# Kernel optimization log

Hardware: AMD Instinct MI355X
Metric: run time of the kernel (lower is better)

## Reference

```python
import jax, jax.numpy as jnp
import numpy as np

B, S, D, FD = 2, 2048, 1024, 4096
EPS_LN = 1e-5


def _l2norm(x):
    n = jnp.linalg.norm(x, axis=-1, keepdims=True)
    return x / jnp.maximum(n, 1e-12)


def _layernorm(x, w, b):
    m = x.mean(-1, keepdims=True)
    v = ((x - m) ** 2).mean(-1, keepdims=True)
    return (x - m) / jnp.sqrt(v + EPS_LN) * w + b


def _spl(x, mu_w, mu_b, gate, proto):
    # cosine-similarity gated linear (SparseProtoLinear)
    scores = _l2norm(x) @ _l2norm(proto).T          # [..., out]
    rw = jax.nn.relu(scores - gate)
    comp = x @ mu_w.T + mu_b
    return comp * rw


def _rotate_half(x):
    h = x.shape[-1] // 2
    return jnp.concatenate([-x[..., h:], x[..., :h]], axis=-1)


def _forward(x, cos, sin,
             ln1_w, ln1_b, ln2_w, ln2_b,
             qkv_mu, qkv_proto, qkv_bias, qkv_gate,
             o_mu, o_proto, o_bias, o_gate,
             f1_mu, f1_proto, f1_bias, f1_gate,
             f2_mu, f2_proto, f2_bias, f2_gate,
             pt_qkv, pt_o, pt_f1, pt_f2,
             pln_qkv_w, pln_qkv_b, pln_o_w, pln_o_b,
             pln_f1_w, pln_f1_b, pln_f2_w, pln_f2_b,
             prev_qkv, prev_o, prev_f1, prev_f2):
    # effective protos: proto_weight + LN(Linear(prev_proto))
    eff_qkv = qkv_proto + _layernorm(prev_qkv @ pt_qkv.T, pln_qkv_w, pln_qkv_b)
    eff_o   = o_proto   + _layernorm(prev_o   @ pt_o.T,   pln_o_w,   pln_o_b)
    eff_f1  = f1_proto  + _layernorm(prev_f1  @ pt_f1.T,  pln_f1_w,  pln_f1_b)
    eff_f2  = f2_proto  + _layernorm(prev_f2  @ pt_f2.T,  pln_f2_w,  pln_f2_b)

    # attention
    attn_in = _layernorm(x, ln1_w, ln1_b)
    m_qkv = _spl(attn_in, qkv_mu, qkv_bias, qkv_gate, eff_qkv)   # [B,S,3D]
    q, k, v = jnp.split(m_qkv, 3, axis=-1)
    c = cos[None]; s = sin[None]
    q = q * c + _rotate_half(q) * s
    k = k * c + _rotate_half(k) * s
    scale = 1.0 / jnp.sqrt(jnp.asarray(D, x.dtype))
    scores = jnp.einsum('bqd,bkd->bqk', q, k) * scale            # [B,S,S]
    causal = jnp.tril(jnp.ones((S, S), dtype=bool))
    scores = jnp.where(causal[None], scores, jnp.finfo(x.dtype).min)
    attn = jax.nn.softmax(scores, axis=-1)
    attn_out = jnp.einsum('bqk,bkd->bqd', attn, v)
    m_o = _spl(attn_out, o_mu, o_bias, o_gate, eff_o)
    x1 = x + m_o

    # ffn (DynamicInfiniteExpert)
    ffn_in = _layernorm(x1, ln2_w, ln2_b)
    m1 = _spl(ffn_in, f1_mu, f1_bias, f1_gate, eff_f1)           # [B,S,FD]
    h = jax.nn.relu(m1)
    m2 = _spl(h, f2_mu, f2_bias, f2_gate, eff_f2)                # [B,S,D]
    return x1 + m2


def setup_inputs() -> dict:
    key = jax.random.key(0)
    ks = iter(jax.random.split(key, 64))

    def nrm(shape, scale=1.0):
        return jax.random.normal(next(ks), shape, dtype=jnp.float32) * scale

    # RoPE tables
    pos = np.arange(S, dtype=np.float32)
    inv_freq = 1.0 / (10000.0 ** (np.arange(0, D, 2, dtype=np.float32) / D))
    freqs = np.outer(pos, inv_freq)
    emb = np.concatenate([freqs, freqs], axis=-1)
    cos = jnp.asarray(np.cos(emb)); sin = jnp.asarray(np.sin(emb))

    sD = 1.0 / np.sqrt(D); sF = 1.0 / np.sqrt(FD)
    inp = {
        'x': nrm((B, S, D)), 'cos': cos, 'sin': sin,
        'ln1_w': jnp.ones((D,)), 'ln1_b': jnp.zeros((D,)),
        'ln2_w': jnp.ones((D,)), 'ln2_b': jnp.zeros((D,)),
        'qkv_mu': nrm((3 * D, D), sD), 'qkv_proto': nrm((3 * D, D), sD),
        'qkv_bias': jnp.zeros((3 * D,)), 'qkv_gate': jnp.zeros((3 * D,)),
        'o_mu': nrm((D, D), sD), 'o_proto': nrm((D, D), sD),
        'o_bias': jnp.zeros((D,)), 'o_gate': jnp.zeros((D,)),
        'f1_mu': nrm((FD, D), sD), 'f1_proto': nrm((FD, D), sD),
        'f1_bias': jnp.zeros((FD,)), 'f1_gate': jnp.zeros((FD,)),
        'f2_mu': nrm((D, FD), sF), 'f2_proto': nrm((D, FD), sF),
        'f2_bias': jnp.zeros((D,)), 'f2_gate': jnp.zeros((D,)),
        'pt_qkv': nrm((D, D), sD), 'pt_o': nrm((D, D), sD),
        'pt_f1': nrm((D, D), sD), 'pt_f2': nrm((FD, FD), sF),
        'pln_qkv_w': jnp.ones((D,)), 'pln_qkv_b': jnp.zeros((D,)),
        'pln_o_w': jnp.ones((D,)), 'pln_o_b': jnp.zeros((D,)),
        'pln_f1_w': jnp.ones((D,)), 'pln_f1_b': jnp.zeros((D,)),
        'pln_f2_w': jnp.ones((FD,)), 'pln_f2_b': jnp.zeros((FD,)),
        'prev_qkv': nrm((3 * D, D), sD), 'prev_o': nrm((D, D), sD),
        'prev_f1': nrm((FD, D), sD), 'prev_f2': nrm((D, FD), sF),
    }
    return inp


def reference(x, cos, sin,
              ln1_w, ln1_b, ln2_w, ln2_b,
              qkv_mu, qkv_proto, qkv_bias, qkv_gate,
              o_mu, o_proto, o_bias, o_gate,
              f1_mu, f1_proto, f1_bias, f1_gate,
              f2_mu, f2_proto, f2_bias, f2_gate,
              pt_qkv, pt_o, pt_f1, pt_f2,
              pln_qkv_w, pln_qkv_b, pln_o_w, pln_o_b,
              pln_f1_w, pln_f1_b, pln_f2_w, pln_f2_b,
              prev_qkv, prev_o, prev_f1, prev_f2):
    return _forward(x, cos, sin, ln1_w, ln1_b, ln2_w, ln2_b,
                    qkv_mu, qkv_proto, qkv_bias, qkv_gate,
                    o_mu, o_proto, o_bias, o_gate,
                    f1_mu, f1_proto, f1_bias, f1_gate,
                    f2_mu, f2_proto, f2_bias, f2_gate,
                    pt_qkv, pt_o, pt_f1, pt_f2,
                    pln_qkv_w, pln_qkv_b, pln_o_w, pln_o_b,
                    pln_f1_w, pln_f1_b, pln_f2_w, pln_f2_b,
                    prev_qkv, prev_o, prev_f1, prev_f2)
```

## Files before the change

### kernel.cpp

```cpp
#include <hip/hip_runtime.h>
#include <cstdint>

typedef unsigned short u16;
typedef __attribute__((ext_vector_type(8))) short sh8;
typedef __attribute__((ext_vector_type(4))) float f32x4;

struct __align__(8) us4 { u16 x, y, z, w; };

__device__ __forceinline__ u16 f2bf(float f) {
  unsigned u = __float_as_uint(f);
  u += 0x7FFFu + ((u >> 16) & 1u);
  return (u16)(u >> 16);
}
__device__ __forceinline__ float bf2f(u16 h) {
  return __uint_as_float((unsigned)h << 16);
}

__device__ __forceinline__ float blk_sum(float v, float* red) {
#pragma unroll
  for (int o = 32; o; o >>= 1) v += __shfl_xor(v, o);
  __syncthreads();
  if ((threadIdx.x & 63) == 0) red[threadIdx.x >> 6] = v;
  __syncthreads();
  return red[0] + red[1] + red[2] + red[3];
}
__device__ __forceinline__ float blk_max(float v, float* red) {
#pragma unroll
  for (int o = 32; o; o >>= 1) v = fmaxf(v, __shfl_xor(v, o));
  __syncthreads();
  if ((threadIdx.x & 63) == 0) red[threadIdx.x >> 6] = v;
  __syncthreads();
  return fmaxf(fmaxf(red[0], red[1]), fmaxf(red[2], red[3]));
}

__global__ void cvt_bf16(const float* __restrict__ S, u16* __restrict__ D, long n4) {
  long i = (long)blockIdx.x * blockDim.x + threadIdx.x;
  if (i >= n4) return;
  float4 v = ((const float4*)S)[i];
  us4 o; o.x = f2bf(v.x); o.y = f2bf(v.y); o.z = f2bf(v.z); o.w = f2bf(v.w);
  ((us4*)D)[i] = o;
}

__global__ void fillv(float* __restrict__ o, long n, float v) {
  long i = (long)blockIdx.x * blockDim.x + threadIdx.x;
  if (i < n) o[i] = v;
}

template <typename CT>
__global__ __launch_bounds__(256, 2) void gemm_bt(
    const u16* __restrict__ A, const u16* __restrict__ B, CT* __restrict__ C,
    int M, int N, int K, int lda, int ldb,
    int mode, long zsA, long zsB, long zsC) {
  int bm, bn;
  int z = blockIdx.z;
  if (mode == 3) {
    int t = blockIdx.x;
    int m = (int)floorf((sqrtf(8.f * t + 1.f) - 1.f) * 0.5f);
    while ((m + 1) * (m + 2) / 2 <= t) ++m;
    while (m * (m + 1) / 2 > t) --m;
    bm = m; bn = t - m * (m + 1) / 2;
  } else {
    bm = blockIdx.x; bn = blockIdx.y;
  }
  int k0s = 0, k0e = K;
  if (mode == 1) {
    int kc = K / gridDim.z;
    k0s = z * kc; k0e = k0s + kc;
    C += (size_t)z * M * (size_t)N;
  } else if (mode >= 2) {
    A += (size_t)z * zsA; B += (size_t)z * zsB; C += (size_t)z * zsC;
  }

  __shared__ __align__(16) u16 As[128 * 32];
  __shared__ __align__(16) u16 Bs[128 * 32];
  int tid = threadIdx.x, wid = tid >> 6, lane = tid & 63;
  int wr = (wid >> 1) << 6, wc = (wid & 1) << 6;
  int lr = lane & 15, lk = (lane >> 4) << 3;

  f32x4 acc[4][4];
  const f32x4 zf = {0.f, 0.f, 0.f, 0.f};
#pragma unroll
  for (int i = 0; i < 4; ++i)
#pragma unroll
    for (int j = 0; j < 4; ++j) acc[i][j] = zf;

  int r0 = tid >> 2, c0 = (tid & 3) << 3;
  const size_t baseA = (size_t)bm * 128, baseB = (size_t)bn * 128;
  const u16* Ab = A + baseA * lda;
  const u16* Bp = B + baseB * ldb;

  for (int k0 = k0s; k0 < k0e; k0 += 32) {
    __builtin_amdgcn_global_load_lds(
        (const __attribute__((address_space(1))) void*)(Ab + (size_t)r0 * lda + k0 + c0),
        (__attribute__((address_space(3))) void*)(As + (wid << 9)), 16, 0, 0);
    __builtin_amdgcn_global_load_lds(
        (const __attribute__((address_space(1))) void*)(Ab + (size_t)(64 + r0) * lda + k0 + c0),
        (__attribute__((address_space(3))) void*)(As + 2048 + (wid << 9)), 16, 0, 0);
    __builtin_amdgcn_global_load_lds(
        (const __attribute__((address_space(1))) void*)(Bp + (size_t)r0 * ldb + k0 + c0),
        (__attribute__((address_space(3))) void*)(Bs + (wid << 9)), 16, 0, 0);
    __builtin_amdgcn_global_load_lds(
        (const __attribute__((address_space(1))) void*)(Bp + (size_t)(64 + r0) * ldb + k0 + c0),
        (__attribute__((address_space(3))) void*)(Bs + 2048 + (wid << 9)), 16, 0, 0);
    __syncthreads();
    sh8 af[4], bfr[4];
#pragma unroll
    for (int f = 0; f < 4; ++f) {
      af[f]  = *(const sh8*)(As + (wr + f * 16 + lr) * 32 + lk);
      bfr[f] = *(const sh8*)(Bs + (wc + f * 16 + lr) * 32 + lk);
    }
#pragma unroll
    for (int i = 0; i < 4; ++i)
#pragma unroll
      for (int j = 0; j < 4; ++j)
        acc[i][j] = __builtin_amdgcn_mfma_f32_16x16x32_bf16(af[i], bfr[j], acc[i][j], 0, 0, 0);
    __syncthreads();
  }

  int cr = (lane >> 4) << 2, cc = lane & 15;
#pragma unroll
  for (int i = 0; i < 4; ++i)
#pragma unroll
    for (int j = 0; j < 4; ++j) {
      size_t cb = (baseA + wr + i * 16 + cr) * (size_t)N + (baseB + wc + j * 16 + cc);
#pragma unroll
      for (int r = 0; r < 4; ++r) {
        float v = acc[i][j][r];
        if constexpr (sizeof(CT) == 2) C[cb + (size_t)r * N] = (CT)f2bf(v);
        else                           C[cb + (size_t)r * N] = v;
      }
    }
}

__global__ void ln_rows(const float* __restrict__ X, const float* __restrict__ w,
                        const float* __restrict__ b, u16* __restrict__ Y,
                        float* __restrict__ norms, int C) {
  __shared__ float red[4];
  int row = blockIdx.x;
  const float* x = X + (size_t)row * C;
  int nv = C >> 2;
  float s = 0.f, ss = 0.f;
  for (int i = threadIdx.x; i < nv; i += 256) {
    float4 v = ((const float4*)x)[i];
    s += v.x + v.y + v.z + v.w;
    ss += v.x * v.x + v.y * v.y + v.z * v.z + v.w * v.w;
  }
  s = blk_sum(s, red);
  ss = blk_sum(ss, red);
  float mean = s / C;
  float inv = rsqrtf(fmaxf(ss / C - mean * mean, 0.f) + 1e-5f);
  float nrm = 0.f;
  for (int i = threadIdx.x; i < nv; i += 256) {
    float4 v = ((const float4*)x)[i];
    float4 wv = ((const float4*)w)[i];
    float4 bv = ((const float4*)b)[i];
    float y0 = (v.x - mean) * inv * wv.x + bv.x;
    float y1 = (v.y - mean) * inv * wv.y + bv.y;
    float y2 = (v.z - mean) * inv * wv.z + bv.z;
    float y3 = (v.w - mean) * inv * wv.w + bv.w;
    nrm += y0 * y0 + y1 * y1 + y2 * y2 + y3 * y3;
    us4 o; o.x = f2bf(y0); o.y = f2bf(y1); o.z = f2bf(y2); o.w = f2bf(y3);
    ((us4*)(Y + (size_t)row * C))[i] = o;
  }
  nrm = blk_sum(nrm, red);
  if (threadIdx.x == 0) norms[row] = fmaxf(sqrtf(nrm), 1e-12f);
}

__global__ void ln_add_norm(const float* __restrict__ T0, const float* __restrict__ T1,
                            const float* __restrict__ P,
                            const float* __restrict__ w, const float* __restrict__ b,
                            u16* __restrict__ E, float* __restrict__ norms, int C) {
  __shared__ float red[4];
  int row = blockIdx.x;
  const float* t0 = T0 + (size_t)row * C;
  const float* t1 = T1 ? T1 + (size_t)row * C : nullptr;
  const float* p = P + (size_t)row * C;
  int nv = C >> 2;
  float s = 0.f, ss = 0.f;
  for (int i = threadIdx.x; i < nv; i += 256) {
    float4 v = ((const float4*)t0)[i];
    if (t1) {
      float4 v1 = ((const float4*)t1)[i];
      v.x += v1.x; v.y += v1.y; v.z += v1.z; v.w += v1.w;
    }
    s += v.x + v.y + v.z + v.w;
    ss += v.x * v.x + v.y * v.y + v.z * v.z + v.w * v.w;
  }
  s = blk_sum(s, red);
  ss = blk_sum(ss, red);
  float mean = s / C;
  float inv = rsqrtf(fmaxf(ss / C - mean * mean, 0.f) + 1e-5f);
  float nrm = 0.f;
  for (int i = threadIdx.x; i < nv; i += 256) {
    float4 v = ((const float4*)t0)[i];
    if (t1) {
      float4 v1 = ((const float4*)t1)[i];
      v.x += v1.x; v.y += v1.y; v.z += v1.z; v.w += v1.w;
    }
    float4 pv = ((const float4*)p)[i];
    float4 wv = ((const float4*)w)[i];
    float4 bv = ((const float4*)b)[i];
    float y0 = pv.x + (v.x - mean) * inv * wv.x + bv.x;
    float y1 = pv.y + (v.y - mean) * inv * wv.y + bv.y;
    float y2 = pv.z + (v.z - mean) * inv * wv.z + bv.z;
    float y3 = pv.w + (v.w - mean) * inv * wv.w + bv.w;
    nrm += y0 * y0 + y1 * y1 + y2 * y2 + y3 * y3;
    us4 o; o.x = f2bf(y0); o.y = f2bf(y1); o.z = f2bf(y2); o.w = f2bf(y3);
    ((us4*)(E + (size_t)row * C))[i] = o;
  }
  nrm = blk_sum(nrm, red);
  if (threadIdx.x == 0) norms[row] = fmaxf(sqrtf(nrm), 1e-12f);
}

__global__ void rownorm_bf(const u16* __restrict__ X, float* __restrict__ norms, int C) {
  __shared__ float red[4];
  int row = blockIdx.x;
  const us4* x = (const us4*)(X + (size_t)row * C);
  int nv = C >> 2;
  float nrm = 0.f;
  for (int i = threadIdx.x; i < nv; i += 256) {
    us4 v = x[i];
    float a = bf2f(v.x), b = bf2f(v.y), c = bf2f(v.z), d = bf2f(v.w);
    nrm += a * a + b * b + c * c + d * d;
  }
  nrm = blk_sum(nrm, red);
  if (threadIdx.x == 0) norms[row] = fmaxf(sqrtf(nrm), 1e-12f);
}

template <typename OT>
__global__ void spl_epi_b(const u16* __restrict__ G, const float* __restrict__ bias,
                          const float* __restrict__ gate, const float* __restrict__ rn,
                          const float* __restrict__ cn, const float* __restrict__ resid,
                          OT* __restrict__ out, int C, int relu_out) {
  int r = blockIdx.x;
  int c = (blockIdx.y << 10) + (threadIdx.x << 2);
  const u16* gr = G + (size_t)r * (2 * C);
  us4 cv = *(const us4*)(gr + c);
  us4 dv = *(const us4*)(gr + C + c);
  float4 bv = *(const float4*)(bias + c);
  float4 gv = *(const float4*)(gate + c);
  float4 nv = *(const float4*)(cn + c);
  float rr = rn[r];
  float cf[4] = {bf2f(cv.x), bf2f(cv.y), bf2f(cv.z), bf2f(cv.w)};
  float df[4] = {bf2f(dv.x), bf2f(dv.y), bf2f(dv.z), bf2f(dv.w)};
  float bb[4] = {bv.x, bv.y, bv.z, bv.w};
  float gg[4] = {gv.x, gv.y, gv.z, gv.w};
  float nn[4] = {nv.x, nv.y, nv.z, nv.w};
  float o[4];
#pragma unroll
  for (int j = 0; j < 4; ++j) {
    float sc = df[j] / (rr * nn[j]);
    float v = (cf[j] + bb[j]) * fmaxf(sc - gg[j], 0.f);
    if (relu_out) v = fmaxf(v, 0.f);
    o[j] = v;
  }
  if (resid) {
    float4 rv = *(const float4*)(resid + (size_t)r * C + c);
    o[0] += rv.x; o[1] += rv.y; o[2] += rv.z; o[3] += rv.w;
  }
  if constexpr (sizeof(OT) == 2) {
    us4 ov; ov.x = f2bf(o[0]); ov.y = f2bf(o[1]); ov.z = f2bf(o[2]); ov.w = f2bf(o[3]);
    *(us4*)((u16*)out + (size_t)r * C + c) = ov;
  } else {
    float4 ov = {o[0], o[1], o[2], o[3]};
    *(float4*)((float*)out + (size_t)r * C + c) = ov;
  }
}

__global__ void spl_epi_p(const float* __restrict__ G0, const float* __restrict__ G1,
                          const float* __restrict__ bias, const float* __restrict__ gate,
                          const float* __restrict__ rn, const float* __restrict__ cn,
                          const float* __restrict__ resid, float* __restrict__ out,
                          int C) {
  int r = blockIdx.x;
  int c = (blockIdx.y << 10) + (threadIdx.x << 2);
  size_t rowb = (size_t)r * (2 * C);
  float4 c0 = *(const float4*)(G0 + rowb + c);
  float4 c1 = *(const float4*)(G1 + rowb + c);
  float4 d0 = *(const float4*)(G0 + rowb + C + c);
  float4 d1 = *(const float4*)(G1 + rowb + C + c);
  float4 bv = *(const float4*)(bias + c);
  float4 gv = *(const float4*)(gate + c);
  float4 nv = *(const float4*)(cn + c);
  float4 rv = *(const float4*)(resid + (size_t)r * C + c);
  float rr = rn[r];
  float cf[4] = {c0.x + c1.x, c0.y + c1.y, c0.z + c1.z, c0.w + c1.w};
  float df[4] = {d0.x + d1.x, d0.y + d1.y, d0.z + d1.z, d0.w + d1.w};
  float bb[4] = {bv.x, bv.y, bv.z, bv.w};
  float gg[4] = {gv.x, gv.y, gv.z, gv.w};
  float nn[4] = {nv.x, nv.y, nv.z, nv.w};
  float re[4] = {rv.x, rv.y, rv.z, rv.w};
  float4 ov;
  float* op = (float*)&ov;
#pragma unroll
  for (int j = 0; j < 4; ++j) {
    float sc = df[j] / (rr * nn[j]);
    op[j] = (cf[j] + bb[j]) * fmaxf(sc - gg[j], 0.f) + re[j];
  }
  *(float4*)(out + (size_t)r * C + c) = ov;
}

__global__ void rope_ip(u16* __restrict__ MQ, const float* __restrict__ CT_,
                        const float* __restrict__ ST_) {
  long t = (long)blockIdx.x * blockDim.x + threadIdx.x;
  int i = (int)(t & 511);
  long row = t >> 9;
  int s = (int)(row & 2047);
  u16* base = MQ + row * 3072;
  float c0 = CT_[(size_t)s * 1024 + i], c1 = CT_[(size_t)s * 1024 + 512 + i];
  float s0 = ST_[(size_t)s * 1024 + i], s1 = ST_[(size_t)s * 1024 + 512 + i];
  float q0 = bf2f(base[i]), q1 = bf2f(base[512 + i]);
  base[i]        = f2bf(q0 * c0 - q1 * s0);
  base[512 + i]  = f2bf(q1 * c1 + q0 * s1);
  float k0 = bf2f(base[1024 + i]), k1 = bf2f(base[1536 + i]);
  base[1024 + i] = f2bf(k0 * c0 - k1 * s0);
  base[1536 + i] = f2bf(k1 * c1 + k0 * s1);
}

__global__ void vtrans(const u16* __restrict__ MQ, u16* __restrict__ VT) {
  __shared__ u16 tile[32][33];
  int b = blockIdx.z;
  int s0 = blockIdx.x << 5, d0 = blockIdx.y << 5;
  int tx = threadIdx.x, ty = threadIdx.y;
  for (int r = ty; r < 32; r += 8)
    tile[r][tx] = MQ[((size_t)(b * 2048 + s0 + r)) * 3072 + 2048 + d0 + tx];
  __syncthreads();
  for (int r = ty; r < 32; r += 8)
    VT[(size_t)b * 1024 * 2048 + (size_t)(d0 + r) * 2048 + s0 + tx] = tile[tx][r];
}

__global__ void softmax_causal(const float* __restrict__ S, u16* __restrict__ P) {
  __shared__ float red[4];
  int b = blockIdx.x >> 11;
  int q = blockIdx.x & 2047;
  const float* row = S + ((size_t)b << 22) + (size_t)q * 2048;
  u16* prow = P + ((size_t)b << 22) + (size_t)q * 2048;
  int nv = q + 1;
  int base = threadIdx.x * 8;
  float xv[8];
  float4 a = *(const float4*)(row + base);
  float4 bq = *(const float4*)(row + base + 4);
  xv[0] = a.x; xv[1] = a.y; xv[2] = a.z; xv[3] = a.w;
  xv[4] = bq.x; xv[5] = bq.y; xv[6] = bq.z; xv[7] = bq.w;
  float m = -3.4e38f;
#pragma unroll
  for (int j = 0; j < 8; ++j) {
    xv[j] *= 0.03125f;
    if (base + j < nv) m = fmaxf(m, xv[j]);
  }
  m = blk_max(m, red);
  float e[8];
  float ssum = 0.f;
#pragma unroll
  for (int j = 0; j < 8; ++j) {
    e[j] = (base + j < nv) ? __expf(xv[j] - m) : 0.f;
    ssum += e[j];
  }
  ssum = blk_sum(ssum, red);
  float invs = 1.f / ssum;
  us4 o;
  o.x = f2bf(e[0] * invs); o.y = f2bf(e[1] * invs);
  o.z = f2bf(e[2] * invs); o.w = f2bf(e[3] * invs);
  ((us4*)prow)[threadIdx.x * 2] = o;
  o.x = f2bf(e[4] * invs); o.y = f2bf(e[5] * invs);
  o.z = f2bf(e[6] * invs); o.w = f2bf(e[7] * invs);
  ((us4*)prow)[threadIdx.x * 2 + 1] = o;
}

extern "C" void kernel_launch(void* const* d_in, const int* in_sizes, int n_in,
                              void* d_out, int out_size, void* d_ws, size_t ws_size,
                              hipStream_t stream) {
  (void)in_sizes;
  const float* x         = (const float*)d_in[0];
  const float* cosT      = (const float*)d_in[1];
  const float* sinT      = (const float*)d_in[2];
  const float* ln1_w     = (const float*)d_in[3];
  const float* ln1_b     = (const float*)d_in[4];
  const float* ln2_w     = (const float*)d_in[5];
  const float* ln2_b     = (const float*)d_in[6];
  const float* qkv_mu    = (const float*)d_in[7];
  const float* qkv_proto = (const float*)d_in[8];
  const float* qkv_bias  = (const float*)d_in[9];
  const float* qkv_gate  = (const float*)d_in[10];
  const float* o_mu      = (const float*)d_in[11];
  const float* o_proto   = (const float*)d_in[12];
  const float* o_bias    = (const float*)d_in[13];
  const float* o_gate    = (const float*)d_in[14];
  const float* f1_mu     = (const float*)d_in[15];
  const float* f1_proto  = (const float*)d_in[16];
  const float* f1_bias   = (const float*)d_in[17];
  const float* f1_gate   = (const float*)d_in[18];
  const float* f2_mu     = (const float*)d_in[19];
  const float* f2_proto  = (const float*)d_in[20];
  const float* f2_bias   = (const float*)d_in[21];
  const float* f2_gate   = (const float*)d_in[22];
  const float* pt_qkv    = (const float*)d_in[23];
  const float* pt_o      = (const float*)d_in[24];
  const float* pt_f1     = (const float*)d_in[25];
  const float* pt_f2     = (const float*)d_in[26];
  const float* pln_qkv_w = (const float*)d_in[27];
  const float* pln_qkv_b = (const float*)d_in[28];
  const float* pln_o_w   = (const float*)d_in[29];
  const float* pln_o_b   = (const float*)d_in[30];
  const float* pln_f1_w  = (const float*)d_in[31];
  const float* pln_f1_b  = (const float*)d_in[32];
  const float* pln_f2_w  = (const float*)d_in[33];
  const float* pln_f2_b  = (const float*)d_in[34];
  const float* prev_qkv  = (const float*)d_in[35];
  const float* prev_o    = (const float*)d_in[36];
  const float* prev_f1   = (const float*)d_in[37];
  const float* prev_f2   = (const float*)d_in[38];

  const long D = 1024, TD = 3072, FD = 4096, R = 4096;

  char* W = (char*)d_ws;
  size_t off = 0;
  auto alloc = [&](size_t bytes) {
    void* p = W + off;
    off = (off + bytes + 255) & ~(size_t)255;
    return p;
  };
  char* GOUT = (char*)alloc(67108864);
  u16*  RC   = (u16*)alloc(33554432);
  u16*  wq   = (u16*)alloc(2 * TD * D * 2);
  u16*  wo   = (u16*)alloc(2 * D * D * 2);
  u16*  wf1  = (u16*)alloc(2 * FD * D * 2);
  u16*  wf2  = (u16*)alloc(2 * D * FD * 2);
  float* X1  = (float*)alloc(R * D * 4);
  float* SC  = (float*)alloc(R * D * 4);
  u16*  P1   = (u16*)alloc(R * D * 2);
  u16*  VT   = (u16*)alloc(2 * D * 2048 * 2);
  u16*  AOB  = (u16*)alloc(R * D * 2);
  float* pnq     = (float*)alloc(TD * 4);
  float* pno     = (float*)alloc(D * 4);
  float* pnf1    = (float*)alloc(FD * 4);
  float* pnf2    = (float*)alloc(D * 4);
  float* rn_ain  = (float*)alloc(R * 4);
  float* rn_aout = (float*)alloc(R * 4);
  float* rn_ffn  = (float*)alloc(R * 4);
  float* rn_h    = (float*)alloc(R * 4);
  size_t need = off;

  if (n_in < 39 || need > ws_size) {
    long n = out_size;
    fillv<<<dim3((unsigned)((n + 255) / 256)), 256, 0, stream>>>((float*)d_out, n, 12345.0f);
    return;
  }

  u16* SA = (u16*)GOUT;
  u16* SB = (u16*)(GOUT + 33554432);
  float* SCORES = (float*)GOUT;
  u16* PB = (u16*)(GOUT + 33554432);

  auto cvt = [&](const float* s, u16* d, long n) {
    long n4 = n >> 2;
    cvt_bf16<<<dim3((unsigned)((n4 + 255) / 256)), 256, 0, stream>>>(s, d, n4);
  };

  struct Proto { const float* prev; const float* pt; const float* proto;
                 const float* w; const float* b; u16* wbuf; float* pn;
                 int M; int N; int K; };
  Proto protos[4] = {
    {prev_qkv, pt_qkv, qkv_proto, pln_qkv_w, pln_qkv_b, wq,  pnq,  3072, 1024, 1024},
    {prev_o,   pt_o,   o_proto,   pln_o_w,   pln_o_b,   wo,  pno,  1024, 1024, 1024},
    {prev_f1,  pt_f1,  f1_proto,  pln_f1_w,  pln_f1_b,  wf1, pnf1, 4096, 1024, 1024},
    {prev_f2,  pt_f2,  f2_proto,  pln_f2_w,  pln_f2_b,  wf2, pnf2, 1024, 4096, 4096},
  };
  for (int p = 0; p < 4; ++p) {
    Proto& pr = protos[p];
    u16* eff = pr.wbuf + (size_t)pr.M * pr.N;
    cvt(pr.prev, SA, (long)pr.M * pr.K);
    cvt(pr.pt,   SB, (long)pr.N * pr.K);
    if (pr.K == 4096) {
      float* T0 = (float*)RC;
      float* T1 = T0 + (size_t)pr.M * pr.N;
      gemm_bt<float><<<dim3(pr.M / 128, pr.N / 128, 2), 256, 0, stream>>>(
          SA, SB, T0, pr.M, pr.N, pr.K, pr.K, pr.K, 1, 0, 0, 0);
      ln_add_norm<<<pr.M, 256, 0, stream>>>(T0, T1, pr.proto, pr.w, pr.b, eff, pr.pn, pr.N);
    } else {
      gemm_bt<float><<<dim3(pr.M / 128, pr.N / 128, 1), 256, 0, stream>>>(
          SA, SB, SC, pr.M, pr.N, pr.K, pr.K, pr.K, 0, 0, 0, 0);
      ln_add_norm<<<pr.M, 256, 0, stream>>>(SC, nullptr, pr.proto, pr.w, pr.b, eff, pr.pn, pr.N);
    }
  }
  cvt(qkv_mu, wq, TD * D);
  cvt(o_mu,   wo, D * D);
  cvt(f1_mu,  wf1, FD * D);
  cvt(f2_mu,  wf2, D * FD);

  ln_rows<<<4096, 256, 0, stream>>>(x, ln1_w, ln1_b, P1, rn_ain, 1024);
  gemm_bt<u16><<<dim3(32, 48, 1), 256, 0, stream>>>(
      P1, wq, (u16*)GOUT, 4096, 6144, 1024, 1024, 1024, 0, 0, 0, 0);
  spl_epi_b<u16><<<dim3(4096, 3), 256, 0, stream>>>(
      (u16*)GOUT, qkv_bias, qkv_gate, rn_ain, pnq, nullptr, RC, 3072, 0);

  rope_ip<<<dim3((unsigned)((R * 512) / 256)), 256, 0, stream>>>(RC, cosT, sinT);
  vtrans<<<dim3(64, 32, 2), dim3(32, 8), 0, stream>>>(RC, VT);
  gemm_bt<float><<<dim3(136, 1, 2), 256, 0, stream>>>(
      RC, RC + 1024, SCORES, 2048, 2048, 1024, 3072, 3072,
      3, 2048L * 3072, 2048L * 3072, 1L << 22);
  softmax_causal<<<4096, 256, 0, stream>>>(SCORES, PB);
  gemm_bt<u16><<<dim3(16, 8, 2), 256, 0, stream>>>(
      PB, VT, AOB, 2048, 1024, 2048, 2048, 2048,
      2, 1L << 22, 1024L * 2048, 2048L * 1024);
  rownorm_bf<<<4096, 256, 0, stream>>>(AOB, rn_aout, 1024);

  gemm_bt<u16><<<dim3(32, 16, 1), 256, 0, stream>>>(
      AOB, wo, (u16*)GOUT, 4096, 2048, 1024, 1024, 1024, 0, 0, 0, 0);
  spl_epi_b<float><<<dim3(4096, 1), 256, 0, stream>>>(
      (u16*)GOUT, o_bias, o_gate, rn_aout, pno, x, X1, 1024, 0);

  ln_rows<<<4096, 256, 0, stream>>>(X1, ln2_w, ln2_b, P1, rn_ffn, 1024);
  gemm_bt<u16><<<dim3(32, 64, 1), 256, 0, stream>>>(
      P1, wf1, (u16*)GOUT, 4096, 8192, 1024, 1024, 1024, 0, 0, 0, 0);
  spl_epi_b<u16><<<dim3(4096, 4), 256, 0, stream>>>(
      (u16*)GOUT, f1_bias, f1_gate, rn_ffn, pnf1, nullptr, RC, 4096, 1);
  rownorm_bf<<<4096, 256, 0, stream>>>(RC, rn_h, 4096);
  gemm_bt<float><<<dim3(32, 16, 2), 256, 0, stream>>>(
      RC, wf2, (float*)GOUT, 4096, 2048, 4096, 4096, 4096, 1, 0, 0, 0);
  spl_epi_p<<<dim3(4096, 1), 256, 0, stream>>>(
      (float*)GOUT, (float*)GOUT + 4096L * 2048, f2_bias, f2_gate, rn_h, pnf2,
      X1, (float*)d_out, 1024);
}
```

Measured before the change: 663.1 us.

## Fuse SPL epilogues with RoPE/LN/rownorm, batch proto GEMMs, skip causal zero blocks

Several changes land together. The QKV epilogue now applies RoPE directly, the O epilogue is fused with the residual add and LN2, and the F1 epilogue computes the row norm. The three K=1024 proto GEMMs are batched into one ragged launch (mode 5), and their intermediate outputs, plus the split-K partials, are stored in bf16 rather than fp32. Causal PV skips the zero K tiles (mode 4), and softmax stops reading and writing masked regions. Together these cut launches and memory traffic, at the cost of some precision from bf16 partial sums.

```diff
diff --git a/kernel.cpp b/kernel.cpp
--- a/kernel.cpp
+++ b/kernel.cpp
@@ -67,8 +67,15 @@
     int kc = K / gridDim.z;
     k0s = z * kc; k0e = k0s + kc;
     C += (size_t)z * M * (size_t)N;
-  } else if (mode >= 2) {
+  } else if (mode == 2 || mode == 3) {
     A += (size_t)z * zsA; B += (size_t)z * zsB; C += (size_t)z * zsC;
+  } else if (mode == 4) {
+    A += (size_t)z * zsA; B += (size_t)z * zsB; C += (size_t)z * zsC;
+    k0e = (bm + 1) * 128;
+  } else if (mode == 5) {
+    int Mz = (int)((zsB >> (z * 16)) & 0xFFFF);
+    if (bm * 128 >= Mz) return;
+    A += (size_t)z * zsA; B += (size_t)z * 1048576; C += (size_t)z * zsC;
   }
 
   __shared__ __align__(16) u16 As[128 * 32];
@@ -166,25 +173,26 @@
   if (threadIdx.x == 0) norms[row] = fmaxf(sqrtf(nrm), 1e-12f);
 }
 
-__global__ void ln_add_norm(const float* __restrict__ T0, const float* __restrict__ T1,
+__global__ void ln_add_norm(const u16* __restrict__ T0, const u16* __restrict__ T1,
                             const float* __restrict__ P,
                             const float* __restrict__ w, const float* __restrict__ b,
                             u16* __restrict__ E, float* __restrict__ norms, int C) {
   __shared__ float red[4];
   int row = blockIdx.x;
-  const float* t0 = T0 + (size_t)row * C;
-  const float* t1 = T1 ? T1 + (size_t)row * C : nullptr;
+  const us4* t0 = (const us4*)(T0 + (size_t)row * C);
+  const us4* t1 = T1 ? (const us4*)(T1 + (size_t)row * C) : nullptr;
   const float* p = P + (size_t)row * C;
   int nv = C >> 2;
   float s = 0.f, ss = 0.f;
   for (int i = threadIdx.x; i < nv; i += 256) {
-    float4 v = ((const float4*)t0)[i];
+    us4 v = t0[i];
+    float f0 = bf2f(v.x), f1 = bf2f(v.y), f2 = bf2f(v.z), f3 = bf2f(v.w);
     if (t1) {
-      float4 v1 = ((const float4*)t1)[i];
-      v.x += v1.x; v.y += v1.y; v.z += v1.z; v.w += v1.w;
+      us4 v1 = t1[i];
+      f0 += bf2f(v1.x); f1 += bf2f(v1.y); f2 += bf2f(v1.z); f3 += bf2f(v1.w);
     }
-    s += v.x + v.y + v.z + v.w;
-    ss += v.x * v.x + v.y * v.y + v.z * v.z + v.w * v.w;
+    s += f0 + f1 + f2 + f3;
+    ss += f0 * f0 + f1 * f1 + f2 * f2 + f3 * f3;
   }
   s = blk_sum(s, red);
   ss = blk_sum(ss, red);
@@ -192,18 +200,19 @@
   float inv = rsqrtf(fmaxf(ss / C - mean * mean, 0.f) + 1e-5f);
   float nrm = 0.f;
   for (int i = threadIdx.x; i < nv; i += 256) {
-    float4 v = ((const float4*)t0)[i];
+    us4 v = t0[i];
+    float f0 = bf2f(v.x), f1 = bf2f(v.y), f2 = bf2f(v.z), f3 = bf2f(v.w);
     if (t1) {
-      float4 v1 = ((const float4*)t1)[i];
-      v.x += v1.x; v.y += v1.y; v.z += v1.z; v.w += v1.w;
+      us4 v1 = t1[i];
+      f0 += bf2f(v1.x); f1 += bf2f(v1.y); f2 += bf2f(v1.z); f3 += bf2f(v1.w);
     }
     float4 pv = ((const float4*)p)[i];
     float4 wv = ((const float4*)w)[i];
     float4 bv = ((const float4*)b)[i];
-    float y0 = pv.x + (v.x - mean) * inv * wv.x + bv.x;
-    float y1 = pv.y + (v.y - mean) * inv * wv.y + bv.y;
-    float y2 = pv.z + (v.z - mean) * inv * wv.z + bv.z;
-    float y3 = pv.w + (v.w - mean) * inv * wv.w + bv.w;
+    float y0 = pv.x + (f0 - mean) * inv * wv.x + bv.x;
+    float y1 = pv.y + (f1 - mean) * inv * wv.y + bv.y;
+    float y2 = pv.z + (f2 - mean) * inv * wv.z + bv.z;
+    float y3 = pv.w + (f3 - mean) * inv * wv.w + bv.w;
     nrm += y0 * y0 + y1 * y1 + y2 * y2 + y3 * y3;
     us4 o; o.x = f2bf(y0); o.y = f2bf(y1); o.z = f2bf(y2); o.w = f2bf(y3);
     ((us4*)(E + (size_t)row * C))[i] = o;
@@ -227,65 +236,154 @@
   if (threadIdx.x == 0) norms[row] = fmaxf(sqrtf(nrm), 1e-12f);
 }
 
-template <typename OT>
-__global__ void spl_epi_b(const u16* __restrict__ G, const float* __restrict__ bias,
-                          const float* __restrict__ gate, const float* __restrict__ rn,
-                          const float* __restrict__ cn, const float* __restrict__ resid,
-                          OT* __restrict__ out, int C, int relu_out) {
-  int r = blockIdx.x;
-  int c = (blockIdx.y << 10) + (threadIdx.x << 2);
-  const u16* gr = G + (size_t)r * (2 * C);
+__device__ __forceinline__ void epi4(const u16* gr, int C, int c, float rr,
+                                     const float* bias, const float* gate,
+                                     const float* cn, float* o) {
   us4 cv = *(const us4*)(gr + c);
   us4 dv = *(const us4*)(gr + C + c);
   float4 bv = *(const float4*)(bias + c);
   float4 gv = *(const float4*)(gate + c);
   float4 nv = *(const float4*)(cn + c);
-  float rr = rn[r];
   float cf[4] = {bf2f(cv.x), bf2f(cv.y), bf2f(cv.z), bf2f(cv.w)};
   float df[4] = {bf2f(dv.x), bf2f(dv.y), bf2f(dv.z), bf2f(dv.w)};
   float bb[4] = {bv.x, bv.y, bv.z, bv.w};
   float gg[4] = {gv.x, gv.y, gv.z, gv.w};
   float nn[4] = {nv.x, nv.y, nv.z, nv.w};
-  float o[4];
 #pragma unroll
   for (int j = 0; j < 4; ++j) {
     float sc = df[j] / (rr * nn[j]);
-    float v = (cf[j] + bb[j]) * fmaxf(sc - gg[j], 0.f);
-    if (relu_out) v = fmaxf(v, 0.f);
-    o[j] = v;
-  }
-  if (resid) {
-    float4 rv = *(const float4*)(resid + (size_t)r * C + c);
-    o[0] += rv.x; o[1] += rv.y; o[2] += rv.z; o[3] += rv.w;
-  }
-  if constexpr (sizeof(OT) == 2) {
+    o[j] = (cf[j] + bb[j]) * fmaxf(sc - gg[j], 0.f);
+  }
+}
+
+__global__ void spl_rope_row(const u16* __restrict__ G, const float* __restrict__ bias,
+                             const float* __restrict__ gate, const float* __restrict__ rn,
+                             const float* __restrict__ cn, const float* __restrict__ CT_,
+                             const float* __restrict__ ST_, u16* __restrict__ MQ) {
+  int r = blockIdx.x;
+  int s = r & 2047;
+  const u16* gr = G + (size_t)r * 6144;
+  u16* outr = MQ + (size_t)r * 3072;
+  float rr = rn[r];
+  int t = threadIdx.x;
+
+  int qk = (t >> 7);
+  int c = qk * 1024 + ((t & 127) << 2);
+  int d = c - qk * 1024;
+  float a0[4], a1[4];
+  epi4(gr, 3072, c, rr, bias, gate, cn, a0);
+  epi4(gr, 3072, c + 512, rr, bias, gate, cn, a1);
+  const float* ct = CT_ + (size_t)s * 1024;
+  const float* st = ST_ + (size_t)s * 1024;
+  float4 c0 = *(const float4*)(ct + d);
+  float4 s0 = *(const float4*)(st + d);
+  float4 c1 = *(const float4*)(ct + d + 512);
+  float4 s1 = *(const float4*)(st + d + 512);
+  float cc0[4] = {c0.x, c0.y, c0.z, c0.w}, ss0[4] = {s0.x, s0.y, s0.z, s0.w};
+  float cc1[4] = {c1.x, c1.y, c1.z, c1.w}, ss1[4] = {s1.x, s1.y, s1.z, s1.w};
+  us4 o0, o1;
+  o0.x = f2bf(a0[0] * cc0[0] - a1[0] * ss0[0]);
+  o0.y = f2bf(a0[1] * cc0[1] - a1[1] * ss0[1]);
+  o0.z = f2bf(a0[2] * cc0[2] - a1[2] * ss0[2]);
+  o0.w = f2bf(a0[3] * cc0[3] - a1[3] * ss0[3]);
+  o1.x = f2bf(a1[0] * cc1[0] + a0[0] * ss1[0]);
+  o1.y = f2bf(a1[1] * cc1[1] + a0[1] * ss1[1]);
+  o1.z = f2bf(a1[2] * cc1[2] + a0[2] * ss1[2]);
+  o1.w = f2bf(a1[3] * cc1[3] + a0[3] * ss1[3]);
+  *(us4*)(outr + c) = o0;
+  *(us4*)(outr + c + 512) = o1;
+
+  int cv_ = 2048 + (t << 2);
+  float vv[4];
+  epi4(gr, 3072, cv_, rr, bias, gate, cn, vv);
+  us4 ov; ov.x = f2bf(vv[0]); ov.y = f2bf(vv[1]); ov.z = f2bf(vv[2]); ov.w = f2bf(vv[3]);
+  *(us4*)(outr + cv_) = ov;
+}
+
+__global__ void spl_f1_row(const u16* __restrict__ G, const float* __restrict__ bias,
+                           const float* __restrict__ gate, const float* __restrict__ rn,
+                           const float* __restrict__ cn, u16* __restrict__ H,
+                           float* __restrict__ rn_h) {
+  __shared__ float red[4];
+  int r = blockIdx.x;
+  const u16* gr = G + (size_t)r * 8192;
+  u16* hr = H + (size_t)r * 4096;
+  float rr = rn[r];
+  float nrm = 0.f;
+  for (int c = threadIdx.x << 2; c < 4096; c += 1024) {
+    float o[4];
+    epi4(gr, 4096, c, rr, bias, gate, cn, o);
+#pragma unroll
+    for (int j = 0; j < 4; ++j) {
+      o[j] = fmaxf(o[j], 0.f);
+      nrm += o[j] * o[j];
+    }
     us4 ov; ov.x = f2bf(o[0]); ov.y = f2bf(o[1]); ov.z = f2bf(o[2]); ov.w = f2bf(o[3]);
-    *(us4*)((u16*)out + (size_t)r * C + c) = ov;
-  } else {
-    float4 ov = {o[0], o[1], o[2], o[3]};
-    *(float4*)((float*)out + (size_t)r * C + c) = ov;
-  }
-}
-
-__global__ void spl_epi_p(const float* __restrict__ G0, const float* __restrict__ G1,
+    *(us4*)(hr + c) = ov;
+  }
+  nrm = blk_sum(nrm, red);
+  if (threadIdx.x == 0) rn_h[r] = fmaxf(sqrtf(nrm), 1e-12f);
+}
+
+__global__ void spl_o_ln_row(const u16* __restrict__ G, const float* __restrict__ bias,
+                             const float* __restrict__ gate, const float* __restrict__ rn,
+                             const float* __restrict__ cn, const float* __restrict__ xres,
+                             const float* __restrict__ lw, const float* __restrict__ lb,
+                             float* __restrict__ X1, u16* __restrict__ Y,
+                             float* __restrict__ rn_ffn) {
+  __shared__ float red[4];
+  int r = blockIdx.x;
+  int c = threadIdx.x << 2;
+  const u16* gr = G + (size_t)r * 2048;
+  float o[4];
+  epi4(gr, 1024, c, rn[r], bias, gate, cn, o);
+  float4 rv = *(const float4*)(xres + (size_t)r * 1024 + c);
+  o[0] += rv.x; o[1] += rv.y; o[2] += rv.z; o[3] += rv.w;
+  float4 xo = {o[0], o[1], o[2], o[3]};
+  *(float4*)(X1 + (size_t)r * 1024 + c) = xo;
+  float s = o[0] + o[1] + o[2] + o[3];
+  float ss = o[0] * o[0] + o[1] * o[1] + o[2] * o[2] + o[3] * o[3];
+  s = blk_sum(s, red);
+  ss = blk_sum(ss, red);
+  float mean = s * (1.f / 1024.f);
+  float inv = rsqrtf(fmaxf(ss * (1.f / 1024.f) - mean * mean, 0.f) + 1e-5f);
+  float4 wv = *(const float4*)(lw + c);
+  float4 bv = *(const float4*)(lb + c);
+  float ww[4] = {wv.x, wv.y, wv.z, wv.w}, bb[4] = {bv.x, bv.y, bv.z, bv.w};
+  float nrm = 0.f;
+  us4 ov;
+  u16* op = (u16*)&ov;
+#pragma unroll
+  for (int j = 0; j < 4; ++j) {
+    float y = (o[j] - mean) * inv * ww[j] + bb[j];
+    nrm += y * y;
+    op[j] = f2bf(y);
+  }
+  *(us4*)(Y + (size_t)r * 1024 + c) = ov;
+  nrm = blk_sum(nrm, red);
+  if (threadIdx.x == 0) rn_ffn[r] = fmaxf(sqrtf(nrm), 1e-12f);
+}
+
+__global__ void spl_epi_p(const u16* __restrict__ G0, const u16* __restrict__ G1,
                           const float* __restrict__ bias, const float* __restrict__ gate,
                           const float* __restrict__ rn, const float* __restrict__ cn,
-                          const float* __restrict__ resid, float* __restrict__ out,
-                          int C) {
+                          const float* __restrict__ resid, float* __restrict__ out) {
   int r = blockIdx.x;
-  int c = (blockIdx.y << 10) + (threadIdx.x << 2);
-  size_t rowb = (size_t)r * (2 * C);
-  float4 c0 = *(const float4*)(G0 + rowb + c);
-  float4 c1 = *(const float4*)(G1 + rowb + c);
-  float4 d0 = *(const float4*)(G0 + rowb + C + c);
-  float4 d1 = *(const float4*)(G1 + rowb + C + c);
+  int c = threadIdx.x << 2;
+  size_t rowb = (size_t)r * 2048;
+  us4 c0 = *(const us4*)(G0 + rowb + c);
+  us4 c1 = *(const us4*)(G1 + rowb + c);
+  us4 d0 = *(const us4*)(G0 + rowb + 1024 + c);
+  us4 d1 = *(const us4*)(G1 + rowb + 1024 + c);
   float4 bv = *(const float4*)(bias + c);
   float4 gv = *(const float4*)(gate + c);
   float4 nv = *(const float4*)(cn + c);
-  float4 rv = *(const float4*)(resid + (size_t)r * C + c);
+  float4 rv = *(const float4*)(resid + (size_t)r * 1024 + c);
   float rr = rn[r];
-  float cf[4] = {c0.x + c1.x, c0.y + c1.y, c0.z + c1.z, c0.w + c1.w};
-  float df[4] = {d0.x + d1.x, d0.y + d1.y, d0.z + d1.z, d0.w + d1.w};
+  float cf[4] = {bf2f(c0.x) + bf2f(c1.x), bf2f(c0.y) + bf2f(c1.y),
+                 bf2f(c0.z) + bf2f(c1.z), bf2f(c0.w) + bf2f(c1.w)};
+  float df[4] = {bf2f(d0.x) + bf2f(d1.x), bf2f(d0.y) + bf2f(d1.y),
+                 bf2f(d0.z) + bf2f(d1.z), bf2f(d0.w) + bf2f(d1.w)};
   float bb[4] = {bv.x, bv.y, bv.z, bv.w};
   float gg[4] = {gv.x, gv.y, gv.z, gv.w};
   float nn[4] = {nv.x, nv.y, nv.z, nv.w};
@@ -297,24 +395,7 @@
     float sc = df[j] / (rr * nn[j]);
     op[j] = (cf[j] + bb[j]) * fmaxf(sc - gg[j], 0.f) + re[j];
   }
-  *(float4*)(out + (size_t)r * C + c) = ov;
-}
-
-__global__ void rope_ip(u16* __restrict__ MQ, const float* __restrict__ CT_,
-                        const float* __restrict__ ST_) {
-  long t = (long)blockIdx.x * blockDim.x + threadIdx.x;
-  int i = (int)(t & 511);
-  long row = t >> 9;
-  int s = (int)(row & 2047);
-  u16* base = MQ + row * 3072;
-  float c0 = CT_[(size_t)s * 1024 + i], c1 = CT_[(size_t)s * 1024 + 512 + i];
-  float s0 = ST_[(size_t)s * 1024 + i], s1 = ST_[(size_t)s * 1024 + 512 + i];
-  float q0 = bf2f(base[i]), q1 = bf2f(base[512 + i]);
-  base[i]        = f2bf(q0 * c0 - q1 * s0);
-  base[512 + i]  = f2bf(q1 * c1 + q0 * s1);
-  float k0 = bf2f(base[1024 + i]), k1 = bf2f(base[1536 + i]);
-  base[1024 + i] = f2bf(k0 * c0 - k1 * s0);
-  base[1536 + i] = f2bf(k1 * c1 + k0 * s1);
+  *(float4*)(out + (size_t)r * 1024 + c) = ov;
 }
 
 __global__ void vtrans(const u16* __restrict__ MQ, u16* __restrict__ VT) {
@@ -336,35 +417,41 @@
   const float* row = S + ((size_t)b << 22) + (size_t)q * 2048;
   u16* prow = P + ((size_t)b << 22) + (size_t)q * 2048;
   int nv = q + 1;
+  int wcap = ((q >> 7) + 1) << 7;
   int base = threadIdx.x * 8;
+  float e[8];
+  float m = -3.4e38f;
   float xv[8];
-  float4 a = *(const float4*)(row + base);
-  float4 bq = *(const float4*)(row + base + 4);
-  xv[0] = a.x; xv[1] = a.y; xv[2] = a.z; xv[3] = a.w;
-  xv[4] = bq.x; xv[5] = bq.y; xv[6] = bq.z; xv[7] = bq.w;
-  float m = -3.4e38f;
+  bool live = base < nv;
+  if (live) {
+    float4 a = *(const float4*)(row + base);
+    float4 bq = *(const float4*)(row + base + 4);
+    xv[0] = a.x; xv[1] = a.y; xv[2] = a.z; xv[3] = a.w;
+    xv[4] = bq.x; xv[5] = bq.y; xv[6] = bq.z; xv[7] = bq.w;
+#pragma unroll
+    for (int j = 0; j < 8; ++j) {
+      xv[j] *= 0.03125f;
+      if (base + j < nv) m = fmaxf(m, xv[j]);
+    }
+  }
+  m = blk_max(m, red);
+  float ssum = 0.f;
 #pragma unroll
   for (int j = 0; j < 8; ++j) {
-    xv[j] *= 0.03125f;
-    if (base + j < nv) m = fmaxf(m, xv[j]);
-  }
-  m = blk_max(m, red);
-  float e[8];
-  float ssum = 0.f;
-#pragma unroll
-  for (int j = 0; j < 8; ++j) {
-    e[j] = (base + j < nv) ? __expf(xv[j] - m) : 0.f;
+    e[j] = (live && base + j < nv) ? __expf(xv[j] - m) : 0.f;
     ssum += e[j];
   }
   ssum = blk_sum(ssum, red);
   float invs = 1.f / ssum;
-  us4 o;
-  o.x = f2bf(e[0] * invs); o.y = f2bf(e[1] * invs);
-  o.z = f2bf(e[2] * invs); o.w = f2bf(e[3] * invs);
-  ((us4*)prow)[threadIdx.x * 2] = o;
-  o.x = f2bf(e[4] * invs); o.y = f2bf(e[5] * invs);
-  o.z = f2bf(e[6] * invs); o.w = f2bf(e[7] * invs);
-  ((us4*)prow)[threadIdx.x * 2 + 1] = o;
+  if (base < wcap) {
+    us4 o;
+    o.x = f2bf(e[0] * invs); o.y = f2bf(e[1] * invs);
+    o.z = f2bf(e[2] * invs); o.w = f2bf(e[3] * invs);
+    ((us4*)prow)[threadIdx.x * 2] = o;
+    o.x = f2bf(e[4] * invs); o.y = f2bf(e[5] * invs);
+    o.z = f2bf(e[6] * invs); o.w = f2bf(e[7] * invs);
+    ((us4*)prow)[threadIdx.x * 2 + 1] = o;
+  }
 }
 
 extern "C" void kernel_launch(void* const* d_in, const int* in_sizes, int n_in,
@@ -427,7 +514,6 @@
   u16*  wf1  = (u16*)alloc(2 * FD * D * 2);
   u16*  wf2  = (u16*)alloc(2 * D * FD * 2);
   float* X1  = (float*)alloc(R * D * 4);
-  float* SC  = (float*)alloc(R * D * 4);
   u16*  P1   = (u16*)alloc(R * D * 2);
   u16*  VT   = (u16*)alloc(2 * D * 2048 * 2);
   u16*  AOB  = (u16*)alloc(R * D * 2);
@@ -448,7 +534,7 @@
   }
 
   u16* SA = (u16*)GOUT;
-  u16* SB = (u16*)(GOUT + 33554432);
+  u16* SB = (u16*)(GOUT + 25165824);
   float* SCORES = (float*)GOUT;
   u16* PB = (u16*)(GOUT + 33554432);
 
@@ -457,32 +543,29 @@
     cvt_bf16<<<dim3((unsigned)((n4 + 255) / 256)), 256, 0, stream>>>(s, d, n4);
   };
 
-  struct Proto { const float* prev; const float* pt; const float* proto;
-                 const float* w; const float* b; u16* wbuf; float* pn;
-                 int M; int N; int K; };
-  Proto protos[4] = {
-    {prev_qkv, pt_qkv, qkv_proto, pln_qkv_w, pln_qkv_b, wq,  pnq,  3072, 1024, 1024},
-    {prev_o,   pt_o,   o_proto,   pln_o_w,   pln_o_b,   wo,  pno,  1024, 1024, 1024},
-    {prev_f1,  pt_f1,  f1_proto,  pln_f1_w,  pln_f1_b,  wf1, pnf1, 4096, 1024, 1024},
-    {prev_f2,  pt_f2,  f2_proto,  pln_f2_w,  pln_f2_b,  wf2, pnf2, 1024, 4096, 4096},
-  };
-  for (int p = 0; p < 4; ++p) {
-    Proto& pr = protos[p];
-    u16* eff = pr.wbuf + (size_t)pr.M * pr.N;
-    cvt(pr.prev, SA, (long)pr.M * pr.K);
-    cvt(pr.pt,   SB, (long)pr.N * pr.K);
-    if (pr.K == 4096) {
-      float* T0 = (float*)RC;
-      float* T1 = T0 + (size_t)pr.M * pr.N;
-      gemm_bt<float><<<dim3(pr.M / 128, pr.N / 128, 2), 256, 0, stream>>>(
-          SA, SB, T0, pr.M, pr.N, pr.K, pr.K, pr.K, 1, 0, 0, 0);
-      ln_add_norm<<<pr.M, 256, 0, stream>>>(T0, T1, pr.proto, pr.w, pr.b, eff, pr.pn, pr.N);
-    } else {
-      gemm_bt<float><<<dim3(pr.M / 128, pr.N / 128, 1), 256, 0, stream>>>(
-          SA, SB, SC, pr.M, pr.N, pr.K, pr.K, pr.K, 0, 0, 0, 0);
-      ln_add_norm<<<pr.M, 256, 0, stream>>>(SC, nullptr, pr.proto, pr.w, pr.b, eff, pr.pn, pr.N);
-    }
-  }
+  cvt(prev_f1,  SA,            FD * D);
+  cvt(prev_qkv, SA + 4194304,  TD * D);
+  cvt(prev_o,   SA + 8388608,  D * D);
+  cvt(pt_f1,    SB,            D * D);
+  cvt(pt_qkv,   SB + 1048576,  D * D);
+  cvt(pt_o,     SB + 2097152,  D * D);
+  {
+    long Mz = 4096L | (3072L << 16) | (1024L << 32);
+    gemm_bt<u16><<<dim3(32, 8, 3), 256, 0, stream>>>(
+        SA, SB, RC, 4096, 1024, 1024, 1024, 1024, 5, 4194304, Mz, 4194304);
+  }
+  ln_add_norm<<<4096, 256, 0, stream>>>(RC, nullptr, f1_proto, pln_f1_w, pln_f1_b,
+                                        wf1 + (size_t)FD * D, pnf1, 1024);
+  ln_add_norm<<<3072, 256, 0, stream>>>(RC + 4194304, nullptr, qkv_proto, pln_qkv_w,
+                                        pln_qkv_b, wq + (size_t)TD * D, pnq, 1024);
+  ln_add_norm<<<1024, 256, 0, stream>>>(RC + 8388608, nullptr, o_proto, pln_o_w,
+                                        pln_o_b, wo + (size_t)D * D, pno, 1024);
+  cvt(prev_f2, SA, D * FD);
+  cvt(pt_f2,   SB, (long)FD * FD);
+  gemm_bt<u16><<<dim3(8, 32, 2), 256, 0, stream>>>(
+      SA, SB, RC, 1024, 4096, 4096, 4096, 4096, 1, 0, 0, 0);
+  ln_add_norm<<<1024, 256, 0, stream>>>(RC, RC + 4194304, f2_proto, pln_f2_w, pln_f2_b,
+                                        wf2 + (size_t)D * FD, pnf2, 4096);
   cvt(qkv_mu, wq, TD * D);
   cvt(o_mu,   wo, D * D);
   cvt(f1_mu,  wf1, FD * D);
@@ -491,10 +574,9 @@
   ln_rows<<<4096, 256, 0, stream>>>(x, ln1_w, ln1_b, P1, rn_ain, 1024);
   gemm_bt<u16><<<dim3(32, 48, 1), 256, 0, stream>>>(
       P1, wq, (u16*)GOUT, 4096, 6144, 1024, 1024, 1024, 0, 0, 0, 0);
-  spl_epi_b<u16><<<dim3(4096, 3), 256, 0, stream>>>(
-      (u16*)GOUT, qkv_bias, qkv_gate, rn_ain, pnq, nullptr, RC, 3072, 0);
-
-  rope_ip<<<dim3((unsigned)((R * 512) / 256)), 256, 0, stream>>>(RC, cosT, sinT);
+  spl_rope_row<<<4096, 256, 0, stream>>>(
+      (u16*)GOUT, qkv_bias, qkv_gate, rn_ain, pnq, cosT, sinT, RC);
+
   vtrans<<<dim3(64, 32, 2), dim3(32, 8), 0, stream>>>(RC, VT);
   gemm_bt<float><<<dim3(136, 1, 2), 256, 0, stream>>>(
       RC, RC + 1024, SCORES, 2048, 2048, 1024, 3072, 3072,
@@ -502,23 +584,21 @@
   softmax_causal<<<4096, 256, 0, stream>>>(SCORES, PB);
   gemm_bt<u16><<<dim3(16, 8, 2), 256, 0, stream>>>(
       PB, VT, AOB, 2048, 1024, 2048, 2048, 2048,
-      2, 1L << 22, 1024L * 2048, 2048L * 1024);
+      4, 1L << 22, 1024L * 2048, 2048L * 1024);
   rownorm_bf<<<4096, 256, 0, stream>>>(AOB, rn_aout, 1024);
 
   gemm_bt<u16><<<dim3(32, 16, 1), 256, 0, stream>>>(
       AOB, wo, (u16*)GOUT, 4096, 2048, 1024, 1024, 1024, 0, 0, 0, 0);
-  spl_epi_b<float><<<dim3(4096, 1), 256, 0, stream>>>(
-      (u16*)GOUT, o_bias, o_gate, rn_aout, pno, x, X1, 1024, 0);
-
-  ln_rows<<<4096, 256, 0, stream>>>(X1, ln2_w, ln2_b, P1, rn_ffn, 1024);
+  spl_o_ln_row<<<4096, 256, 0, stream>>>(
+      (u16*)GOUT, o_bias, o_gate, rn_aout, pno, x, ln2_w, ln2_b, X1, P1, rn_ffn);
+
   gemm_bt<u16><<<dim3(32, 64, 1), 256, 0, stream>>>(
       P1, wf1, (u16*)GOUT, 4096, 8192, 1024, 1024, 1024, 0, 0, 0, 0);
-  spl_epi_b<u16><<<dim3(4096, 4), 256, 0, stream>>>(
-      (u16*)GOUT, f1_bias, f1_gate, rn_ffn, pnf1, nullptr, RC, 4096, 1);
-  rownorm_bf<<<4096, 256, 0, stream>>>(RC, rn_h, 4096);
-  gemm_bt<float><<<dim3(32, 16, 2), 256, 0, stream>>>(
-      RC, wf2, (float*)GOUT, 4096, 2048, 4096, 4096, 4096, 1, 0, 0, 0);
-  spl_epi_p<<<dim3(4096, 1), 256, 0, stream>>>(
-      (float*)GOUT, (float*)GOUT + 4096L * 2048, f2_bias, f2_gate, rn_h, pnf2,
-      X1, (float*)d_out, 1024);
-}
+  spl_f1_row<<<4096, 256, 0, stream>>>(
+      (u16*)GOUT, f1_bias, f1_gate, rn_ffn, pnf1, RC, rn_h);
+  gemm_bt<u16><<<dim3(32, 16, 2), 256, 0, stream>>>(
+      RC, wf2, (u16*)GOUT, 4096, 2048, 4096, 4096, 4096, 1, 0, 0, 0);
+  spl_epi_p<<<4096, 256, 0, stream>>>(
+      (u16*)GOUT, (u16*)GOUT + 8388608, f2_bias, f2_gate, rn_h, pnf2,
+      X1, (float*)d_out);
+}
```

New measurement: 596.0 us. 10.1% less time.
